# Performance work log

Measured on AMD Instinct MI355X. Metric: run time of the kernel, lower is better.

Reference implementation:

```python
import jax, jax.numpy as jnp
import numpy as np

N_TEXT = 80000
N_NON = 20000
N = N_TEXT + N_NON
E = 200000
EMB = 256
HID = 256
R = 500
V = 17
MDIM = 64
K = 4
NUM_ROUNDS = 2
NUM_REV_ROUNDS = 2


def setup_inputs():
    key = jax.random.key(0)
    ks = jax.random.split(key, 32)
    f = jnp.float32
    s = 0.05
    inp = {}
    inp["h_id_tensor"] = jax.random.randint(ks[0], (E,), 0, N)
    inp["r_id_tensor"] = jax.random.randint(ks[1], (E,), 0, R)
    inp["t_id_tensor"] = jax.random.randint(ks[2], (E,), 0, N)
    inp["q_emb"] = jax.random.normal(ks[3], (1, EMB), f)
    inp["entity_embs"] = jax.random.normal(ks[4], (N_TEXT, EMB), f)
    inp["num_non_text_entities"] = N_NON
    inp["relation_embs"] = jax.random.normal(ks[5], (R, EMB), f)
    inp["topic_entity_one_hot"] = (jax.random.uniform(ks[6], (N, 2)) < 0.01).astype(f)
    inp["node_motif_token_ids"] = jax.random.randint(ks[7], (N, K), 0, V)
    inp["node_motif_token_wts"] = jax.random.uniform(ks[8], (N, K), f)
    inp["triple_motif_token_ids"] = jax.random.randint(ks[9], (E, K), 0, V)
    inp["triple_motif_token_wts"] = jax.random.uniform(ks[10], (E, K), f)
    inp["non_text_emb"] = jax.random.normal(ks[11], (EMB,), f) * s
    me = jax.random.normal(ks[12], (V, MDIM), f) * s
    inp["motif_emb"] = me.at[0].set(0.0)  # padding_idx=0
    inp["gnn_self_w"] = jax.random.normal(ks[13], (MDIM, MDIM), f) * s
    inp["gnn_self_b"] = jnp.zeros((MDIM,), f)
    inp["gnn_msg_w"] = jax.random.normal(ks[14], (MDIM, MDIM), f) * s
    inp["gnn_msg_b"] = jnp.zeros((MDIM,), f)
    pos_dim = 2 + 2 * (NUM_ROUNDS + NUM_REV_ROUNDS)  # 10
    inp["nh_w"] = jax.random.normal(ks[15], (2 * EMB + 2 * MDIM, HID), f) * s
    inp["nh_b"] = jnp.zeros((HID,), f)
    inp["pos_w"] = jax.random.normal(ks[16], (2 * pos_dim, HID), f) * s
    inp["pos_b"] = jnp.zeros((HID,), f)
    inp["st_w"] = jax.random.normal(ks[17], (EMB + MDIM, HID), f) * s
    inp["st_b"] = jnp.zeros((HID,), f)
    inp["gate_w"] = jax.random.normal(ks[18], (EMB, 3), f) * s
    inp["gate_b"] = jnp.zeros((3,), f)
    inp["pred_w1"] = jax.random.normal(ks[19], (EMB + HID, HID), f) * s
    inp["pred_b1"] = jnp.zeros((HID,), f)
    inp["pred_w2"] = jax.random.normal(ks[20], (HID, 1), f) * s
    inp["pred_b2"] = jnp.zeros((1,), f)
    return inp


def _forward(h_id, r_id, t_id, q_emb, entity_embs, num_non_text, relation_embs,
             topic_oh, node_ids, node_wts, trip_ids, trip_wts,
             non_text_emb, motif_emb, gsw, gsb, gmw, gmb,
             nh_w, nh_b, pos_w, pos_b, st_w, st_b, gate_w, gate_b,
             pw1, pb1, pw2, pb2):
    n = entity_embs.shape[0] + num_non_text
    h_e = jnp.concatenate(
        [entity_embs,
         jnp.broadcast_to(non_text_emb[None, :], (num_non_text, entity_embs.shape[1]))],
        axis=0)  # [N, EMB]
    ones = jnp.ones((h_id.shape[0],), h_e.dtype)
    inv_fwd = 1.0 / jnp.clip(jax.ops.segment_sum(ones, t_id, num_segments=n), 1.0)[:, None]
    inv_rev = 1.0 / jnp.clip(jax.ops.segment_sum(ones, h_id, num_segments=n), 1.0)[:, None]

    def mean_agg(x, src, dst, inv):
        # PyG mean aggregation: mean of source features over incoming edges, 0 if none
        return jax.ops.segment_sum(x[src], dst, num_segments=n) * inv

    dde_list = []
    h = topic_oh
    for _ in range(NUM_ROUNDS):
        h = mean_agg(h, h_id, t_id, inv_fwd)
        dde_list.append(h)
    h = topic_oh
    for _ in range(NUM_REV_ROUNDS):
        h = mean_agg(h, t_id, h_id, inv_rev)
        dde_list.append(h)

    # ---- motif co-occurrence adjacency (vectorized form of the K x K loop) ----
    contrib = trip_wts[:, :, None] * trip_wts[:, None, :]                 # [E,K,K]
    valid = (trip_ids[:, :, None] > 0) & (trip_ids[:, None, :] > 0) & (contrib > 0)
    contrib = jnp.where(valid, contrib, 0.0)
    idx = (trip_ids[:, :, None] * V + trip_ids[:, None, :]).reshape(-1)
    adj = jnp.zeros((V * V,), contrib.dtype).at[idx].add(contrib.reshape(-1)).reshape(V, V)
    adj = 0.5 * (adj + adj.T) + jnp.eye(V, dtype=adj.dtype)
    adj = adj.at[0, :].set(0.0).at[:, 0].set(0.0).at[0, 0].set(1.0)
    adj = adj / jnp.clip(adj.sum(axis=1, keepdims=True), 1e-8)

    # ---- semantic GNN over the motif table ----
    ht = motif_emb
    for _ in range(1):  # semantic_gnn_num_layers = 1, dropout 0 (eval)
        msg = adj @ ht
        ht = ht + jax.nn.relu(ht @ gsw + gsb + msg @ gmw + gmb)

    node_motif_emb = (ht[node_ids] * node_wts[:, :, None]).sum(axis=1)    # [N,MDIM]
    triple_motif_emb = (ht[trip_ids] * trip_wts[:, :, None]).sum(axis=1)  # [E,MDIM]

    h_r = relation_embs[r_id]                                             # [E,EMB]
    h_nbr = jax.nn.relu(
        jnp.concatenate([h_e[h_id], h_e[t_id], node_motif_emb[h_id], node_motif_emb[t_id]],
                        axis=1) @ nh_w + nh_b)
    pos_feat = jnp.concatenate([topic_oh] + dde_list, axis=1)             # [N,10]
    h_pos = jax.nn.relu(
        jnp.concatenate([pos_feat[h_id], pos_feat[t_id]], axis=1) @ pos_w + pos_b)
    h_str = jax.nn.relu(jnp.concatenate([h_r, triple_motif_emb], axis=1) @ st_w + st_b)

    gate = jax.nn.softmax((q_emb @ gate_w + gate_b)[0])                   # [3]
    h_fused = gate[0] * h_nbr + gate[1] * h_pos + gate[2] * h_str
    pred_in = jnp.concatenate(
        [jnp.broadcast_to(q_emb, (h_r.shape[0], q_emb.shape[1])), h_fused], axis=1)
    return jax.nn.relu(pred_in @ pw1 + pb1) @ pw2 + pb2                   # [E,1]


def reference(h_id_tensor, r_id_tensor, t_id_tensor, q_emb, entity_embs,
              num_non_text_entities, relation_embs, topic_entity_one_hot,
              node_motif_token_ids, node_motif_token_wts,
              triple_motif_token_ids, triple_motif_token_wts,
              non_text_emb, motif_emb, gnn_self_w, gnn_self_b, gnn_msg_w, gnn_msg_b,
              nh_w, nh_b, pos_w, pos_b, st_w, st_b, gate_w, gate_b,
              pred_w1, pred_b1, pred_w2, pred_b2):
    return _forward(h_id_tensor, r_id_tensor, t_id_tensor, q_emb, entity_embs,
                    num_non_text_entities, relation_embs, topic_entity_one_hot,
                    node_motif_token_ids, node_motif_token_wts,
                    triple_motif_token_ids, triple_motif_token_wts,
                    non_text_emb, motif_emb, gnn_self_w, gnn_self_b, gnn_msg_w, gnn_msg_b,
                    nh_w, nh_b, pos_w, pos_b, st_w, st_b, gate_w, gate_b,
                    pred_w1, pred_b1, pred_w2, pred_b2)
```

## Files before the change

### kernel.cpp

```cpp
#include <hip/hip_runtime.h>
#include <hip/hip_bf16.h>

#define N_TEXT 80000
#define NTOT   100000
#define NE     200000
#define EMB    256
#define HID    256
#define VMOT   17
#define MDIM   64
#define KTOK   4

typedef unsigned short u16;
typedef unsigned int   u32;
typedef short short8 __attribute__((ext_vector_type(8)));
typedef float f32x4 __attribute__((ext_vector_type(4)));

#define O_INVF 0
#define O_INVR (NTOT)
#define O_POS  (2*NTOT)
#define O_ADJ  (12*NTOT)
#define O_HTB  (12*NTOT + 512)
#define O_GATE (12*NTOT + 1088)
#define O_CVEC (12*NTOT + 1104)
#define O_NME  (12*NTOT + 1360)
#define O_WSW  (O_NME + NTOT*32)
#define ZERO_FLOATS (12*NTOT + 512)

#define OW_A 0
#define OW_B 163840
#define OW_C 172032
#define OW_D 253952
#define SZ_W 319488
#define GA 20480
#define GB 1024
#define GC 10240
#define GD 8192
#define GTOT (GA+GB+GC+GD)

__device__ __forceinline__ u16 f2b(float f) {
  unsigned u = __float_as_uint(f);
  return (u16)((u + 0x7fffu + ((u >> 16) & 1u)) >> 16);
}
__device__ __forceinline__ float b2f(u16 v) {
  return __uint_as_float(((unsigned)v) << 16);
}
__device__ __forceinline__ short8 pack8(const float* f) {
  short8 v;
#pragma unroll
  for (int j = 0; j < 8; j++) v[j] = (short)f2b(f[j]);
  return v;
}

__global__ void k_zero(float* ws, int n) {
  int i = blockIdx.x * blockDim.x + threadIdx.x;
  if (i < n) ws[i] = 0.f;
}

__global__ void k_prep_w(const float* __restrict__ nh_w, const float* __restrict__ pos_w,
                         const float* __restrict__ st_w, const float* __restrict__ pw1,
                         float* __restrict__ ws) {
  int g = blockIdx.x * blockDim.x + threadIdx.x;
  if (g >= GTOT) return;
  int l, phase;
  if (g < GA) { l = g; phase = 0; }
  else if (g < GA + GB) { l = g - GA; phase = 1; }
  else if (g < GA + GB + GC) { l = g - GA - GB; phase = 2; }
  else { l = g - GA - GB - GC; phase = 3; }
  int c = l >> 10, r = l & 1023;
  int w = r >> 8, nt = (r >> 6) & 3, ln = r & 63;
  int col = w*64 + nt*16 + (ln & 15);
  int k0  = c*32 + ((ln >> 4) << 3);
  float f[8];
#pragma unroll
  for (int j = 0; j < 8; j++) {
    int k = k0 + j;
    float v = 0.f;
    if (phase == 0)      v = nh_w[k*256 + col];
    else if (phase == 1) { if (k < 10) v = pos_w[k*256 + col];
                           else if (k >= 16 && k < 26) v = pos_w[(k-6)*256 + col]; }
    else if (phase == 2) v = st_w[k*256 + col];
    else                 v = pw1[(256 + k)*256 + col];
    f[j] = v;
  }
  ((short8*)((u16*)(ws + O_WSW)))[g] = pack8(f);
}

__global__ void k_deg_dde1(const int* __restrict__ h_id, const int* __restrict__ t_id,
                           const float* __restrict__ topic, float* __restrict__ ws) {
  int e = blockIdx.x * blockDim.x + threadIdx.x;
  if (e >= NE) return;
  int h = h_id[e], t = t_id[e];
  atomicAdd(&ws[O_INVF + t], 1.0f);
  atomicAdd(&ws[O_INVR + h], 1.0f);
  float hx = topic[2*h], hy = topic[2*h + 1];
  float tx = topic[2*t], ty = topic[2*t + 1];
  if (hx != 0.f) atomicAdd(&ws[O_POS + t*10 + 2], hx);
  if (hy != 0.f) atomicAdd(&ws[O_POS + t*10 + 3], hy);
  if (tx != 0.f) atomicAdd(&ws[O_POS + h*10 + 6], tx);
  if (ty != 0.f) atomicAdd(&ws[O_POS + h*10 + 7], ty);
}

__global__ void k_prep_nodes(const float* __restrict__ topic, float* __restrict__ ws) {
  int n = blockIdx.x * blockDim.x + threadIdx.x;
  if (n >= NTOT) return;
  float invf = 1.0f / fmaxf(ws[O_INVF + n], 1.0f);
  float invr = 1.0f / fmaxf(ws[O_INVR + n], 1.0f);
  ws[O_INVF + n] = invf;
  ws[O_INVR + n] = invr;
  float* p = &ws[O_POS + n*10];
  p[0] = topic[2*n]; p[1] = topic[2*n + 1];
  p[2] *= invf; p[3] *= invf;
  p[6] *= invr; p[7] *= invr;
}

__global__ void k_dde2(const int* __restrict__ h_id, const int* __restrict__ t_id,
                       float* __restrict__ ws) {
  int e = blockIdx.x * blockDim.x + threadIdx.x;
  if (e >= NE) return;
  int h = h_id[e], t = t_id[e];
  float a = ws[O_POS + h*10 + 2], b = ws[O_POS + h*10 + 3];
  float c = ws[O_POS + t*10 + 6], d = ws[O_POS + t*10 + 7];
  if (a != 0.f) atomicAdd(&ws[O_POS + t*10 + 4], a);
  if (b != 0.f) atomicAdd(&ws[O_POS + t*10 + 5], b);
  if (c != 0.f) atomicAdd(&ws[O_POS + h*10 + 8], c);
  if (d != 0.f) atomicAdd(&ws[O_POS + h*10 + 9], d);
}

__global__ void k_dde2_scale(float* __restrict__ ws) {
  int n = blockIdx.x * blockDim.x + threadIdx.x;
  if (n >= NTOT) return;
  float invf = ws[O_INVF + n], invr = ws[O_INVR + n];
  float* p = &ws[O_POS + n*10];
  p[4] *= invf; p[5] *= invf;
  p[8] *= invr; p[9] *= invr;
}

__global__ void k_adj(const int* __restrict__ tids, const float* __restrict__ twts,
                      float* __restrict__ ws) {
  __shared__ float sadj[4*304];
  for (int i = threadIdx.x; i < 4*304; i += blockDim.x) sadj[i] = 0.f;
  __syncthreads();
  int wbase = (threadIdx.x >> 6) * 304;
  int e = blockIdx.x * blockDim.x + threadIdx.x;
  if (e < NE) {
    int id[KTOK]; float w[KTOK];
#pragma unroll
    for (int k = 0; k < KTOK; k++) { id[k] = tids[e*KTOK + k]; w[k] = twts[e*KTOK + k]; }
#pragma unroll
    for (int i = 0; i < KTOK; i++)
#pragma unroll
      for (int j = 0; j < KTOK; j++) {
        float c = w[i] * w[j];
        if (id[i] > 0 && id[j] > 0 && c > 0.f)
          atomicAdd(&sadj[wbase + id[i]*VMOT + id[j]], c);
      }
  }
  __syncthreads();
  for (int i = threadIdx.x; i < VMOT*VMOT; i += blockDim.x) {
    float v = sadj[i] + sadj[304 + i] + sadj[608 + i] + sadj[912 + i];
    if (v != 0.f) atomicAdd(&ws[O_ADJ + i], v);
  }
}

__global__ void k_motif_gate(const float* __restrict__ mo, const float* __restrict__ gsw,
                             const float* __restrict__ gsb, const float* __restrict__ gmw,
                             const float* __restrict__ gmb, const float* __restrict__ q,
                             const float* __restrict__ gate_w, const float* __restrict__ gate_b,
                             const float* __restrict__ pw1, const float* __restrict__ pb1,
                             float* __restrict__ ws) {
  int t = threadIdx.x;
  if (blockIdx.x == 0) {
    __shared__ float A[VMOT*VMOT];
    __shared__ float Bm[VMOT*VMOT];
    __shared__ float inv_row[VMOT];
    __shared__ float smo[VMOT*MDIM];
    __shared__ float sm[VMOT*MDIM];
    for (int i = t; i < VMOT*VMOT; i += blockDim.x) A[i] = ws[O_ADJ + i];
    for (int i = t; i < VMOT*MDIM; i += blockDim.x) smo[i] = mo[i];
    __syncthreads();
    for (int i = t; i < VMOT*VMOT; i += blockDim.x) {
      int r = i / VMOT, c = i % VMOT;
      float v = 0.5f * (A[i] + A[c*VMOT + r]) + (r == c ? 1.f : 0.f);
      if (r == 0 || c == 0) v = (r == 0 && c == 0) ? 1.f : 0.f;
      Bm[i] = v;
    }
    __syncthreads();
    if (t < VMOT) {
      float s = 0.f;
      for (int c = 0; c < VMOT; c++) s += Bm[t*VMOT + c];
      inv_row[t] = 1.f / fmaxf(s, 1e-8f);
    }
    __syncthreads();
    for (int i = t; i < VMOT*MDIM; i += blockDim.x) {
      int v = i / MDIM, d = i % MDIM;
      float s = 0.f;
      for (int u = 0; u < VMOT; u++) s += Bm[v*VMOT + u] * smo[u*MDIM + d];
      sm[i] = s * inv_row[v];
    }
    __syncthreads();
    for (int i = t; i < VMOT*MDIM; i += blockDim.x) {
      int v = i / MDIM, d = i % MDIM;
      float a = gsb[d] + gmb[d];
      for (int m = 0; m < MDIM; m++)
        a += smo[v*MDIM + m] * gsw[m*MDIM + d] + sm[v*MDIM + m] * gmw[m*MDIM + d];
      ((u16*)(ws + O_HTB))[i] = f2b(smo[i] + fmaxf(a, 0.f));
    }
  } else {
    __shared__ float sq[EMB];
    __shared__ float red[3];
    sq[t] = q[t];
    if (t < 3) red[t] = 0.f;
    __syncthreads();
    float s = pb1[t];
    for (int i = 0; i < EMB; i++) s += sq[i] * pw1[i*HID + t];
    ws[O_CVEC + t] = s;
    atomicAdd(&red[0], sq[t] * gate_w[t*3 + 0]);
    atomicAdd(&red[1], sq[t] * gate_w[t*3 + 1]);
    atomicAdd(&red[2], sq[t] * gate_w[t*3 + 2]);
    __syncthreads();
    if (t == 0) {
      float l0 = red[0] + gate_b[0], l1 = red[1] + gate_b[1], l2 = red[2] + gate_b[2];
      float mx = fmaxf(l0, fmaxf(l1, l2));
      float e0 = expf(l0 - mx), e1 = expf(l1 - mx), e2 = expf(l2 - mx);
      float inv = 1.f / (e0 + e1 + e2);
      ws[O_GATE + 0] = e0 * inv; ws[O_GATE + 1] = e1 * inv; ws[O_GATE + 2] = e2 * inv;
    }
  }
}

__global__ void k_nme(const int* __restrict__ nids, const float* __restrict__ nwts,
                      float* __restrict__ ws) {
  __shared__ u16 sht[VMOT*MDIM];
  for (int i = threadIdx.x; i < (VMOT*MDIM)/2; i += blockDim.x)
    ((u32*)sht)[i] = ((const u32*)(ws + O_HTB))[i];
  __syncthreads();
  int gid = blockIdx.x * blockDim.x + threadIdx.x;
  if (gid >= NTOT * 8) return;
  int n = gid >> 3, d0 = (gid & 7) * 8;
  int4   iv = ((const int4*)nids)[n];
  float4 wv = ((const float4*)nwts)[n];
  int   id[4] = {iv.x, iv.y, iv.z, iv.w};
  float w[4]  = {wv.x, wv.y, wv.z, wv.w};
  float f[8];
#pragma unroll
  for (int j = 0; j < 8; j++) {
    float s = 0.f;
#pragma unroll
    for (int k = 0; k < 4; k++) s += w[k] * b2f(sht[id[k]*MDIM + d0 + j]);
    f[j] = s;
  }
  ((short8*)((u16*)(ws + O_NME)))[gid] = pack8(f);
}

__global__ __launch_bounds__(256, 2) void k_edge_mfma(
    const int* __restrict__ h_id, const int* __restrict__ r_id, const int* __restrict__ t_id,
    const float* __restrict__ ent, const float* __restrict__ rel, const float* __restrict__ nte,
    const int* __restrict__ tids, const float* __restrict__ twts,
    const float* __restrict__ nh_b, const float* __restrict__ pos_b,
    const float* __restrict__ st_b, const float* __restrict__ pw2,
    const float* __restrict__ pb2,
    const float* __restrict__ ws, float* __restrict__ out) {
  __shared__ __align__(16) u16 sX[64*32];
  __shared__ __align__(16) u16 sW[8192];
  __shared__ __align__(16) u16 sF[8*64*32];
  __shared__ float sOut[64];
  __shared__ int sh[64], stt[64], sr[64];

  const int tid = threadIdx.x;
  const int wv = tid >> 6, ln = tid & 63;
  const int lm = ln & 15, lq = ln >> 4;
  const int cb = wv * 64;
  const int e0 = blockIdx.x * 64;
  const int srow = tid >> 2, sks = tid & 3;

  if (tid < 64) {
    sh[tid]  = h_id[e0 + tid];
    stt[tid] = t_id[e0 + tid];
    sr[tid]  = r_id[e0 + tid];
    sOut[tid] = 0.f;
  }
  const float g0 = ws[O_GATE + 0], g1 = ws[O_GATE + 1], g2 = ws[O_GATE + 2];
  const u16* Wsw = (const u16*)(ws + O_WSW);
  const u16* WA = Wsw + OW_A;
  const u16* WB = Wsw + OW_B;
  const u16* WC = Wsw + OW_C;
  const u16* WD = Wsw + OW_D;
  const u16* nmeb = (const u16*)(ws + O_NME);
  const u16* htb  = (const u16*)(ws + O_HTB);
  const int4   tiv = ((const int4*)tids)[e0 + srow];
  const float4 twv = ((const float4*)twts)[e0 + srow];
  __syncthreads();

  f32x4 acc[4][4];
  float fused[4][4][4];
#pragma unroll
  for (int mt = 0; mt < 4; mt++)
#pragma unroll
    for (int nt = 0; nt < 4; nt++) {
      acc[mt][nt] = (f32x4){0.f, 0.f, 0.f, 0.f};
#pragma unroll
      for (int r = 0; r < 4; r++) fused[mt][nt][r] = 0.f;
    }

#define LOADW(W, c)                                                      \
  { const u16* p = (W) + (c)*8192 + tid*8;                               \
    wreg[0] = *(const short8*)(p);                                       \
    wreg[1] = *(const short8*)(p + 2048);                                \
    wreg[2] = *(const short8*)(p + 4096);                                \
    wreg[3] = *(const short8*)(p + 6144); }

#define STOREW()                                                         \
  { *(short8*)&sW[tid*8]        = wreg[0];                               \
    *(short8*)&sW[2048 + tid*8] = wreg[1];                               \
    *(short8*)&sW[4096 + tid*8] = wreg[2];                               \
    *(short8*)&sW[6144 + tid*8] = wreg[3]; }

#define MFMA_STEP()                                                      \
  { short8 a[4], b[4];                                                   \
    _Pragma("unroll")                                                    \
    for (int mt = 0; mt < 4; mt++)                                       \
      a[mt] = *(const short8*)&sX[(mt*16 + lm)*32 + lq*8];               \
    _Pragma("unroll")                                                    \
    for (int nt = 0; nt < 4; nt++)                                       \
      b[nt] = *(const short8*)&sW[wv*2048 + nt*512 + ln*8];              \
    _Pragma("unroll")                                                    \
    for (int mt = 0; mt < 4; mt++)                                       \
      _Pragma("unroll")                                                  \
      for (int nt = 0; nt < 4; nt++)                                     \
        acc[mt][nt] = __builtin_amdgcn_mfma_f32_16x16x32_bf16(a[mt], b[nt], acc[mt][nt], 0, 0, 0); }

  short8 wreg[4];

  {
    float4 fa, fb; short8 xs;
    auto loadA = [&](int kc) {
      int kk = kc + sks*8;
      if (kk < 512) {
        int node = (kk < 256) ? sh[srow] : stt[srow];
        int k2 = kk & 255;
        const float* src = (node < N_TEXT) ? &ent[(size_t)node*256 + k2] : &nte[k2];
        fa = *(const float4*)src; fb = *(const float4*)(src + 4);
      } else {
        int node = (kk < 576) ? sh[srow] : stt[srow];
        xs = *(const short8*)&nmeb[node*64 + ((kk - 512) & 63)];
      }
    };
    loadA(0); LOADW(WA, 0);
    for (int c = 0; c < 20; c++) {
      if (c*32 < 512) {
        float f[8] = {fa.x, fa.y, fa.z, fa.w, fb.x, fb.y, fb.z, fb.w};
        *(short8*)&sX[srow*32 + sks*8] = pack8(f);
      } else {
        *(short8*)&sX[srow*32 + sks*8] = xs;
      }
      STOREW();
      __syncthreads();
      if (c < 19) { loadA((c+1)*32); LOADW(WA, c+1); }
      MFMA_STEP();
      __syncthreads();
    }
  }
#pragma unroll
  for (int nt = 0; nt < 4; nt++) {
    float bb = nh_b[cb + nt*16 + lm];
#pragma unroll
    for (int mt = 0; mt < 4; mt++)
#pragma unroll
      for (int r = 0; r < 4; r++) {
        fused[mt][nt][r] += g0 * fmaxf(acc[mt][nt][r] + bb, 0.f);
        acc[mt][nt][r] = 0.f;
      }
  }

  {
    LOADW(WB, 0);
    int node_h = sh[srow], node_t = stt[srow];
    float f[8];
#pragma unroll
    for (int j = 0; j < 8; j++) {
      int kk = sks*8 + j;
      float v = 0.f;
      if (kk < 10) v = ws[O_POS + node_h*10 + kk];
      else if (kk >= 16 && kk < 26) v = ws[O_POS + node_t*10 + kk - 16];
      f[j] = v;
    }
    *(short8*)&sX[srow*32 + sks*8] = pack8(f);
    STOREW();
    __syncthreads();
    MFMA_STEP();
    __syncthreads();
  }
#pragma unroll
  for (int nt = 0; nt < 4; nt++) {
    float bb = pos_b[cb + nt*16 + lm];
#pragma unroll
    for (int mt = 0; mt < 4; mt++)
#pragma unroll
      for (int r = 0; r < 4; r++) {
        fused[mt][nt][r] += g1 * fmaxf(acc[mt][nt][r] + bb, 0.f);
        acc[mt][nt][r] = 0.f;
      }
  }

  {
    float4 fa, fb; short8 hs0, hs1, hs2, hs3;
    auto loadC = [&](int kc) {
      int kk = kc + sks*8;
      if (kk < 256) {
        const float* src = &rel[(size_t)sr[srow]*256 + kk];
        fa = *(const float4*)src; fb = *(const float4*)(src + 4);
      } else {
        int d0 = kk - 256;
        hs0 = *(const short8*)&htb[tiv.x*64 + d0];
        hs1 = *(const short8*)&htb[tiv.y*64 + d0];
        hs2 = *(const short8*)&htb[tiv.z*64 + d0];
        hs3 = *(const short8*)&htb[tiv.w*64 + d0];
      }
    };
    loadC(0); LOADW(WC, 0);
    for (int c = 0; c < 10; c++) {
      if (c < 8) {
        float f[8] = {fa.x, fa.y, fa.z, fa.w, fb.x, fb.y, fb.z, fb.w};
        *(short8*)&sX[srow*32 + sks*8] = pack8(f);
      } else {
        float f[8];
#pragma unroll
        for (int j = 0; j < 8; j++)
          f[j] = twv.x * b2f((u16)hs0[j]) + twv.y * b2f((u16)hs1[j])
               + twv.z * b2f((u16)hs2[j]) + twv.w * b2f((u16)hs3[j]);
        *(short8*)&sX[srow*32 + sks*8] = pack8(f);
      }
      STOREW();
      __syncthreads();
      if (c < 9) { loadC((c+1)*32); LOADW(WC, c+1); }
      MFMA_STEP();
      __syncthreads();
    }
  }
#pragma unroll
  for (int nt = 0; nt < 4; nt++) {
    float bb = st_b[cb + nt*16 + lm];
#pragma unroll
    for (int mt = 0; mt < 4; mt++)
#pragma unroll
      for (int r = 0; r < 4; r++) {
        fused[mt][nt][r] += g2 * fmaxf(acc[mt][nt][r] + bb, 0.f);
        acc[mt][nt][r] = 0.f;
      }
  }

  LOADW(WD, 0);
#pragma unroll
  for (int mt = 0; mt < 4; mt++)
#pragma unroll
    for (int nt = 0; nt < 4; nt++) {
      int col = cb + nt*16 + lm;
      int base = (col >> 5)*2048 + (col & 31);
#pragma unroll
      for (int r = 0; r < 4; r++)
        sF[base + (mt*16 + lq*4 + r)*32] = f2b(fused[mt][nt][r]);
    }

  for (int c = 0; c < 8; c++) {
    STOREW();
    __syncthreads();
    if (c < 7) LOADW(WD, c+1);
    {
      short8 a[4], b[4];
#pragma unroll
      for (int mt = 0; mt < 4; mt++)
        a[mt] = *(const short8*)&sF[c*2048 + (mt*16 + lm)*32 + lq*8];
#pragma unroll
      for (int nt = 0; nt < 4; nt++)
        b[nt] = *(const short8*)&sW[wv*2048 + nt*512 + ln*8];
#pragma unroll
      for (int mt = 0; mt < 4; mt++)
#pragma unroll
        for (int nt = 0; nt < 4; nt++)
          acc[mt][nt] = __builtin_amdgcn_mfma_f32_16x16x32_bf16(a[mt], b[nt], acc[mt][nt], 0, 0, 0);
    }
    __syncthreads();
  }

  {
    float cv[4], p2[4];
#pragma unroll
    for (int nt = 0; nt < 4; nt++) {
      int col = cb + nt*16 + lm;
      cv[nt] = ws[O_CVEC + col];
      p2[nt] = pw2[col];
    }
#pragma unroll
    for (int mt = 0; mt < 4; mt++)
#pragma unroll
      for (int r = 0; r < 4; r++) {
        float s = 0.f;
#pragma unroll
        for (int nt = 0; nt < 4; nt++)
          s += fmaxf(acc[mt][nt][r] + cv[nt], 0.f) * p2[nt];
#pragma unroll
        for (int off = 1; off < 16; off <<= 1)
          s += __shfl_xor(s, off, 64);
        if (lm == 0) atomicAdd(&sOut[mt*16 + lq*4 + r], s);
      }
  }
  __syncthreads();
  if (tid < 64) out[e0 + tid] = sOut[tid] + pb2[0];
#undef LOADW
#undef STOREW
#undef MFMA_STEP
}

extern "C" void kernel_launch(void* const* d_in, const int* in_sizes, int n_in,
                              void* d_out, int out_size, void* d_ws, size_t ws_size,
                              hipStream_t stream) {
  (void)in_sizes; (void)n_in; (void)out_size; (void)ws_size;
  const int*   h_id   = (const int*)  d_in[0];
  const int*   r_id   = (const int*)  d_in[1];
  const int*   t_id   = (const int*)  d_in[2];
  const float* q      = (const float*)d_in[3];
  const float* ent    = (const float*)d_in[4];
  const float* rel    = (const float*)d_in[6];
  const float* topic  = (const float*)d_in[7];
  const int*   nids   = (const int*)  d_in[8];
  const float* nwts   = (const float*)d_in[9];
  const int*   tids   = (const int*)  d_in[10];
  const float* twts   = (const float*)d_in[11];
  const float* nte    = (const float*)d_in[12];
  const float* mo     = (const float*)d_in[13];
  const float* gsw    = (const float*)d_in[14];
  const float* gsb    = (const float*)d_in[15];
  const float* gmw    = (const float*)d_in[16];
  const float* gmb    = (const float*)d_in[17];
  const float* nh_w   = (const float*)d_in[18];
  const float* nh_b   = (const float*)d_in[19];
  const float* pos_w  = (const float*)d_in[20];
  const float* pos_b  = (const float*)d_in[21];
  const float* st_w   = (const float*)d_in[22];
  const float* st_b   = (const float*)d_in[23];
  const float* gate_w = (const float*)d_in[24];
  const float* gate_b = (const float*)d_in[25];
  const float* pw1    = (const float*)d_in[26];
  const float* pb1    = (const float*)d_in[27];
  const float* pw2    = (const float*)d_in[28];
  const float* pb2    = (const float*)d_in[29];
  float* ws  = (float*)d_ws;
  float* out = (float*)d_out;

  k_zero<<<(ZERO_FLOATS + 255)/256, 256, 0, stream>>>(ws, ZERO_FLOATS);
  k_prep_w<<<(GTOT + 255)/256, 256, 0, stream>>>(nh_w, pos_w, st_w, pw1, ws);
  k_deg_dde1<<<(NE + 255)/256, 256, 0, stream>>>(h_id, t_id, topic, ws);
  k_prep_nodes<<<(NTOT + 255)/256, 256, 0, stream>>>(topic, ws);
  k_dde2<<<(NE + 255)/256, 256, 0, stream>>>(h_id, t_id, ws);
  k_dde2_scale<<<(NTOT + 255)/256, 256, 0, stream>>>(ws);
  k_adj<<<(NE + 255)/256, 256, 0, stream>>>(tids, twts, ws);
  k_motif_gate<<<2, 256, 0, stream>>>(mo, gsw, gsb, gmw, gmb, q, gate_w, gate_b, pw1, pb1, ws);
  k_nme<<<(NTOT*8 + 255)/256, 256, 0, stream>>>(nids, nwts, ws);
  k_edge_mfma<<<NE/64, 256, 0, stream>>>(h_id, r_id, t_id, ent, rel, nte, tids, twts,
                                         nh_b, pos_b, st_b, pw2, pb2, ws, out);
}
```

Before: 533.5 us.

## Fuse preprocessing kernels and load MFMA operands directly from global memory

Result: slower. 710.9 us (+33.2%).

```diff
diff --git a/kernel.cpp b/kernel.cpp
--- a/kernel.cpp
+++ b/kernel.cpp
@@ -25,12 +25,12 @@
 #define O_NME  (12*NTOT + 1360)
 #define O_WSW  (O_NME + NTOT*32)
 #define ZERO_FLOATS (12*NTOT + 512)
+#define Z4 (ZERO_FLOATS/4)
 
 #define OW_A 0
 #define OW_B 163840
 #define OW_C 172032
 #define OW_D 253952
-#define SZ_W 319488
 #define GA 20480
 #define GB 1024
 #define GC 10240
@@ -44,22 +44,22 @@
 __device__ __forceinline__ float b2f(u16 v) {
   return __uint_as_float(((unsigned)v) << 16);
 }
-__device__ __forceinline__ short8 pack8(const float* f) {
-  short8 v;
-#pragma unroll
-  for (int j = 0; j < 8; j++) v[j] = (short)f2b(f[j]);
-  return v;
-}
-
-__global__ void k_zero(float* ws, int n) {
-  int i = blockIdx.x * blockDim.x + threadIdx.x;
-  if (i < n) ws[i] = 0.f;
-}
-
-__global__ void k_prep_w(const float* __restrict__ nh_w, const float* __restrict__ pos_w,
-                         const float* __restrict__ st_w, const float* __restrict__ pw1,
-                         float* __restrict__ ws) {
+__device__ __forceinline__ short8 pack8f(const float* f) {
+  union { u32 u[4]; short8 s; } o;
+#pragma unroll
+  for (int i = 0; i < 4; i++) {
+    __hip_bfloat162 b = __float22bfloat162_rn(float2{f[2*i], f[2*i+1]});
+    o.u[i] = *reinterpret_cast<u32*>(&b);
+  }
+  return o.s;
+}
+
+__global__ void k_prep(const float* __restrict__ nh_w, const float* __restrict__ pos_w,
+                       const float* __restrict__ st_w, const float* __restrict__ pw1,
+                       float* __restrict__ ws) {
   int g = blockIdx.x * blockDim.x + threadIdx.x;
+  if (g < Z4) { ((float4*)ws)[g] = make_float4(0.f, 0.f, 0.f, 0.f); return; }
+  g -= Z4;
   if (g >= GTOT) return;
   int l, phase;
   if (g < GA) { l = g; phase = 0; }
@@ -82,67 +82,28 @@
     else                 v = pw1[(256 + k)*256 + col];
     f[j] = v;
   }
-  ((short8*)((u16*)(ws + O_WSW)))[g] = pack8(f);
-}
-
-__global__ void k_deg_dde1(const int* __restrict__ h_id, const int* __restrict__ t_id,
-                           const float* __restrict__ topic, float* __restrict__ ws) {
-  int e = blockIdx.x * blockDim.x + threadIdx.x;
-  if (e >= NE) return;
-  int h = h_id[e], t = t_id[e];
-  atomicAdd(&ws[O_INVF + t], 1.0f);
-  atomicAdd(&ws[O_INVR + h], 1.0f);
-  float hx = topic[2*h], hy = topic[2*h + 1];
-  float tx = topic[2*t], ty = topic[2*t + 1];
-  if (hx != 0.f) atomicAdd(&ws[O_POS + t*10 + 2], hx);
-  if (hy != 0.f) atomicAdd(&ws[O_POS + t*10 + 3], hy);
-  if (tx != 0.f) atomicAdd(&ws[O_POS + h*10 + 6], tx);
-  if (ty != 0.f) atomicAdd(&ws[O_POS + h*10 + 7], ty);
-}
-
-__global__ void k_prep_nodes(const float* __restrict__ topic, float* __restrict__ ws) {
-  int n = blockIdx.x * blockDim.x + threadIdx.x;
-  if (n >= NTOT) return;
-  float invf = 1.0f / fmaxf(ws[O_INVF + n], 1.0f);
-  float invr = 1.0f / fmaxf(ws[O_INVR + n], 1.0f);
-  ws[O_INVF + n] = invf;
-  ws[O_INVR + n] = invr;
-  float* p = &ws[O_POS + n*10];
-  p[0] = topic[2*n]; p[1] = topic[2*n + 1];
-  p[2] *= invf; p[3] *= invf;
-  p[6] *= invr; p[7] *= invr;
-}
-
-__global__ void k_dde2(const int* __restrict__ h_id, const int* __restrict__ t_id,
-                       float* __restrict__ ws) {
-  int e = blockIdx.x * blockDim.x + threadIdx.x;
-  if (e >= NE) return;
-  int h = h_id[e], t = t_id[e];
-  float a = ws[O_POS + h*10 + 2], b = ws[O_POS + h*10 + 3];
-  float c = ws[O_POS + t*10 + 6], d = ws[O_POS + t*10 + 7];
-  if (a != 0.f) atomicAdd(&ws[O_POS + t*10 + 4], a);
-  if (b != 0.f) atomicAdd(&ws[O_POS + t*10 + 5], b);
-  if (c != 0.f) atomicAdd(&ws[O_POS + h*10 + 8], c);
-  if (d != 0.f) atomicAdd(&ws[O_POS + h*10 + 9], d);
-}
-
-__global__ void k_dde2_scale(float* __restrict__ ws) {
-  int n = blockIdx.x * blockDim.x + threadIdx.x;
-  if (n >= NTOT) return;
-  float invf = ws[O_INVF + n], invr = ws[O_INVR + n];
-  float* p = &ws[O_POS + n*10];
-  p[4] *= invf; p[5] *= invf;
-  p[8] *= invr; p[9] *= invr;
-}
-
-__global__ void k_adj(const int* __restrict__ tids, const float* __restrict__ twts,
-                      float* __restrict__ ws) {
+  ((short8*)((u16*)(ws + O_WSW)))[g] = pack8f(f);
+}
+
+__global__ void k_deg_dde1_adj(const int* __restrict__ h_id, const int* __restrict__ t_id,
+                               const float* __restrict__ topic,
+                               const int* __restrict__ tids, const float* __restrict__ twts,
+                               float* __restrict__ ws) {
   __shared__ float sadj[4*304];
   for (int i = threadIdx.x; i < 4*304; i += blockDim.x) sadj[i] = 0.f;
   __syncthreads();
   int wbase = (threadIdx.x >> 6) * 304;
   int e = blockIdx.x * blockDim.x + threadIdx.x;
   if (e < NE) {
+    int h = h_id[e], t = t_id[e];
+    atomicAdd(&ws[O_INVF + t], 1.0f);
+    atomicAdd(&ws[O_INVR + h], 1.0f);
+    float hx = topic[2*h], hy = topic[2*h + 1];
+    float tx = topic[2*t], ty = topic[2*t + 1];
+    if (hx != 0.f) atomicAdd(&ws[O_POS + t*10 + 2], hx);
+    if (hy != 0.f) atomicAdd(&ws[O_POS + t*10 + 3], hy);
+    if (tx != 0.f) atomicAdd(&ws[O_POS + h*10 + 6], tx);
+    if (ty != 0.f) atomicAdd(&ws[O_POS + h*10 + 7], ty);
     int id[KTOK]; float w[KTOK];
 #pragma unroll
     for (int k = 0; k < KTOK; k++) { id[k] = tids[e*KTOK + k]; w[k] = twts[e*KTOK + k]; }
@@ -162,23 +123,35 @@
   }
 }
 
-__global__ void k_motif_gate(const float* __restrict__ mo, const float* __restrict__ gsw,
-                             const float* __restrict__ gsb, const float* __restrict__ gmw,
-                             const float* __restrict__ gmb, const float* __restrict__ q,
-                             const float* __restrict__ gate_w, const float* __restrict__ gate_b,
-                             const float* __restrict__ pw1, const float* __restrict__ pb1,
-                             float* __restrict__ ws) {
+#define NPN_BLOCKS ((NTOT + 255)/256)
+__global__ void k_pnm(const float* __restrict__ topic, const float* __restrict__ mo,
+                      const float* __restrict__ gsw, const float* __restrict__ gsb,
+                      const float* __restrict__ gmw, const float* __restrict__ gmb,
+                      const float* __restrict__ q, const float* __restrict__ gate_w,
+                      const float* __restrict__ gate_b, const float* __restrict__ pw1,
+                      const float* __restrict__ pb1, float* __restrict__ ws) {
   int t = threadIdx.x;
-  if (blockIdx.x == 0) {
+  if (blockIdx.x < NPN_BLOCKS) {
+    int n = blockIdx.x * 256 + t;
+    if (n >= NTOT) return;
+    float invf = 1.0f / fmaxf(ws[O_INVF + n], 1.0f);
+    float invr = 1.0f / fmaxf(ws[O_INVR + n], 1.0f);
+    ws[O_INVF + n] = invf;
+    ws[O_INVR + n] = invr;
+    float* p = &ws[O_POS + n*10];
+    p[0] = topic[2*n]; p[1] = topic[2*n + 1];
+    p[2] *= invf; p[3] *= invf;
+    p[6] *= invr; p[7] *= invr;
+  } else if (blockIdx.x == NPN_BLOCKS) {
     __shared__ float A[VMOT*VMOT];
     __shared__ float Bm[VMOT*VMOT];
     __shared__ float inv_row[VMOT];
     __shared__ float smo[VMOT*MDIM];
     __shared__ float sm[VMOT*MDIM];
-    for (int i = t; i < VMOT*VMOT; i += blockDim.x) A[i] = ws[O_ADJ + i];
-    for (int i = t; i < VMOT*MDIM; i += blockDim.x) smo[i] = mo[i];
+    for (int i = t; i < VMOT*VMOT; i += 256) A[i] = ws[O_ADJ + i];
+    for (int i = t; i < VMOT*MDIM; i += 256) smo[i] = mo[i];
     __syncthreads();
-    for (int i = t; i < VMOT*VMOT; i += blockDim.x) {
+    for (int i = t; i < VMOT*VMOT; i += 256) {
       int r = i / VMOT, c = i % VMOT;
       float v = 0.5f * (A[i] + A[c*VMOT + r]) + (r == c ? 1.f : 0.f);
       if (r == 0 || c == 0) v = (r == 0 && c == 0) ? 1.f : 0.f;
@@ -191,14 +164,14 @@
       inv_row[t] = 1.f / fmaxf(s, 1e-8f);
     }
     __syncthreads();
-    for (int i = t; i < VMOT*MDIM; i += blockDim.x) {
+    for (int i = t; i < VMOT*MDIM; i += 256) {
       int v = i / MDIM, d = i % MDIM;
       float s = 0.f;
       for (int u = 0; u < VMOT; u++) s += Bm[v*VMOT + u] * smo[u*MDIM + d];
       sm[i] = s * inv_row[v];
     }
     __syncthreads();
-    for (int i = t; i < VMOT*MDIM; i += blockDim.x) {
+    for (int i = t; i < VMOT*MDIM; i += 256) {
       int v = i / MDIM, d = i % MDIM;
       float a = gsb[d] + gmb[d];
       for (int m = 0; m < MDIM; m++)
@@ -228,31 +201,46 @@
   }
 }
 
-__global__ void k_nme(const int* __restrict__ nids, const float* __restrict__ nwts,
-                      float* __restrict__ ws) {
+__global__ void k_dde2(const int* __restrict__ h_id, const int* __restrict__ t_id,
+                       float* __restrict__ ws) {
+  int e = blockIdx.x * blockDim.x + threadIdx.x;
+  if (e >= NE) return;
+  int h = h_id[e], t = t_id[e];
+  float a = ws[O_POS + h*10 + 2], b = ws[O_POS + h*10 + 3];
+  float c = ws[O_POS + t*10 + 6], d = ws[O_POS + t*10 + 7];
+  if (a != 0.f) atomicAdd(&ws[O_POS + t*10 + 4], a);
+  if (b != 0.f) atomicAdd(&ws[O_POS + t*10 + 5], b);
+  if (c != 0.f) atomicAdd(&ws[O_POS + h*10 + 8], c);
+  if (d != 0.f) atomicAdd(&ws[O_POS + h*10 + 9], d);
+}
+
+__global__ void k_scale_nme(const int* __restrict__ nids, const float* __restrict__ nwts,
+                            float* __restrict__ ws) {
   __shared__ u16 sht[VMOT*MDIM];
   for (int i = threadIdx.x; i < (VMOT*MDIM)/2; i += blockDim.x)
     ((u32*)sht)[i] = ((const u32*)(ws + O_HTB))[i];
   __syncthreads();
   int gid = blockIdx.x * blockDim.x + threadIdx.x;
+  if (gid < NTOT) {
+    float invf = ws[O_INVF + gid], invr = ws[O_INVR + gid];
+    float* p = &ws[O_POS + gid*10];
+    p[4] *= invf; p[5] *= invf;
+    p[8] *= invr; p[9] *= invr;
+  }
   if (gid >= NTOT * 8) return;
   int n = gid >> 3, d0 = (gid & 7) * 8;
   int4   iv = ((const int4*)nids)[n];
   float4 wv = ((const float4*)nwts)[n];
-  int   id[4] = {iv.x, iv.y, iv.z, iv.w};
-  float w[4]  = {wv.x, wv.y, wv.z, wv.w};
   float f[8];
 #pragma unroll
   for (int j = 0; j < 8; j++) {
-    float s = 0.f;
-#pragma unroll
-    for (int k = 0; k < 4; k++) s += w[k] * b2f(sht[id[k]*MDIM + d0 + j]);
-    f[j] = s;
-  }
-  ((short8*)((u16*)(ws + O_NME)))[gid] = pack8(f);
-}
-
-__global__ __launch_bounds__(256, 2) void k_edge_mfma(
+    f[j] = wv.x * b2f(sht[iv.x*MDIM + d0 + j]) + wv.y * b2f(sht[iv.y*MDIM + d0 + j])
+         + wv.z * b2f(sht[iv.z*MDIM + d0 + j]) + wv.w * b2f(sht[iv.w*MDIM + d0 + j]);
+  }
+  ((short8*)((u16*)(ws + O_NME)))[gid] = pack8f(f);
+}
+
+__global__ __launch_bounds__(256, 3) void k_edge_mfma(
     const int* __restrict__ h_id, const int* __restrict__ r_id, const int* __restrict__ t_id,
     const float* __restrict__ ent, const float* __restrict__ rel, const float* __restrict__ nte,
     const int* __restrict__ tids, const float* __restrict__ twts,
@@ -260,226 +248,192 @@
     const float* __restrict__ st_b, const float* __restrict__ pw2,
     const float* __restrict__ pb2,
     const float* __restrict__ ws, float* __restrict__ out) {
-  __shared__ __align__(16) u16 sX[64*32];
-  __shared__ __align__(16) u16 sW[8192];
-  __shared__ __align__(16) u16 sF[8*64*32];
+  __shared__ __align__(16) u16 sF[16384];
   __shared__ float sOut[64];
-  __shared__ int sh[64], stt[64], sr[64];
 
   const int tid = threadIdx.x;
   const int wv = tid >> 6, ln = tid & 63;
   const int lm = ln & 15, lq = ln >> 4;
   const int cb = wv * 64;
   const int e0 = blockIdx.x * 64;
-  const int srow = tid >> 2, sks = tid & 3;
-
-  if (tid < 64) {
-    sh[tid]  = h_id[e0 + tid];
-    stt[tid] = t_id[e0 + tid];
-    sr[tid]  = r_id[e0 + tid];
-    sOut[tid] = 0.f;
+
+  if (tid < 64) sOut[tid] = 0.f;
+
+  int nh[4], ntl[4], nr[4];
+#pragma unroll
+  for (int mt = 0; mt < 4; mt++) {
+    int e = e0 + mt*16 + lm;
+    nh[mt] = h_id[e]; ntl[mt] = t_id[e]; nr[mt] = r_id[e];
   }
   const float g0 = ws[O_GATE + 0], g1 = ws[O_GATE + 1], g2 = ws[O_GATE + 2];
-  const u16* Wsw = (const u16*)(ws + O_WSW);
-  const u16* WA = Wsw + OW_A;
-  const u16* WB = Wsw + OW_B;
-  const u16* WC = Wsw + OW_C;
-  const u16* WD = Wsw + OW_D;
+  const u16* blob = (const u16*)(ws + O_WSW);
   const u16* nmeb = (const u16*)(ws + O_NME);
   const u16* htb  = (const u16*)(ws + O_HTB);
-  const int4   tiv = ((const int4*)tids)[e0 + srow];
-  const float4 twv = ((const float4*)twts)[e0 + srow];
-  __syncthreads();
 
   f32x4 acc[4][4];
-  float fused[4][4][4];
 #pragma unroll
   for (int mt = 0; mt < 4; mt++)
 #pragma unroll
-    for (int nt = 0; nt < 4; nt++) {
-      acc[mt][nt] = (f32x4){0.f, 0.f, 0.f, 0.f};
-#pragma unroll
-      for (int r = 0; r < 4; r++) fused[mt][nt][r] = 0.f;
-    }
-
-#define LOADW(W, c)                                                      \
-  { const u16* p = (W) + (c)*8192 + tid*8;                               \
-    wreg[0] = *(const short8*)(p);                                       \
-    wreg[1] = *(const short8*)(p + 2048);                                \
-    wreg[2] = *(const short8*)(p + 4096);                                \
-    wreg[3] = *(const short8*)(p + 6144); }
-
-#define STOREW()                                                         \
-  { *(short8*)&sW[tid*8]        = wreg[0];                               \
-    *(short8*)&sW[2048 + tid*8] = wreg[1];                               \
-    *(short8*)&sW[4096 + tid*8] = wreg[2];                               \
-    *(short8*)&sW[6144 + tid*8] = wreg[3]; }
-
-#define MFMA_STEP()                                                      \
-  { short8 a[4], b[4];                                                   \
-    _Pragma("unroll")                                                    \
-    for (int mt = 0; mt < 4; mt++)                                       \
-      a[mt] = *(const short8*)&sX[(mt*16 + lm)*32 + lq*8];               \
-    _Pragma("unroll")                                                    \
-    for (int nt = 0; nt < 4; nt++)                                       \
-      b[nt] = *(const short8*)&sW[wv*2048 + nt*512 + ln*8];              \
-    _Pragma("unroll")                                                    \
-    for (int mt = 0; mt < 4; mt++)                                       \
-      _Pragma("unroll")                                                  \
-      for (int nt = 0; nt < 4; nt++)                                     \
-        acc[mt][nt] = __builtin_amdgcn_mfma_f32_16x16x32_bf16(a[mt], b[nt], acc[mt][nt], 0, 0, 0); }
-
-  short8 wreg[4];
-
-  {
-    float4 fa, fb; short8 xs;
-    auto loadA = [&](int kc) {
-      int kk = kc + sks*8;
-      if (kk < 512) {
-        int node = (kk < 256) ? sh[srow] : stt[srow];
-        int k2 = kk & 255;
-        const float* src = (node < N_TEXT) ? &ent[(size_t)node*256 + k2] : &nte[k2];
-        fa = *(const float4*)src; fb = *(const float4*)(src + 4);
-      } else {
-        int node = (kk < 576) ? sh[srow] : stt[srow];
-        xs = *(const short8*)&nmeb[node*64 + ((kk - 512) & 63)];
-      }
-    };
-    loadA(0); LOADW(WA, 0);
-    for (int c = 0; c < 20; c++) {
-      if (c*32 < 512) {
-        float f[8] = {fa.x, fa.y, fa.z, fa.w, fb.x, fb.y, fb.z, fb.w};
-        *(short8*)&sX[srow*32 + sks*8] = pack8(f);
-      } else {
-        *(short8*)&sX[srow*32 + sks*8] = xs;
-      }
-      STOREW();
-      __syncthreads();
-      if (c < 19) { loadA((c+1)*32); LOADW(WA, c+1); }
-      MFMA_STEP();
-      __syncthreads();
-    }
+    for (int nt = 0; nt < 4; nt++) acc[mt][nt] = (f32x4){0.f, 0.f, 0.f, 0.f};
+
+  auto bload = [&](int bc, short8 (&b)[4]) {
+#pragma unroll
+    for (int nt = 0; nt < 4; nt++)
+      b[nt] = *(const short8*)&blob[(size_t)bc*8192 + wv*2048 + nt*512 + ln*8];
+  };
+  auto mfma16 = [&](short8 (&a)[4], short8 (&b)[4]) {
+#pragma unroll
+    for (int mt = 0; mt < 4; mt++)
+#pragma unroll
+      for (int nt = 0; nt < 4; nt++)
+        acc[mt][nt] = __builtin_amdgcn_mfma_f32_16x16x32_bf16(a[mt], b[nt], acc[mt][nt], 0, 0, 0);
+  };
+
+#pragma unroll 2
+  for (int c = 0; c < 8; c++) {
+    short8 a[4], b[4];
+#pragma unroll
+    for (int mt = 0; mt < 4; mt++) {
+      int node = nh[mt];
+      const float* p = ((node < N_TEXT) ? &ent[(size_t)node*256] : nte) + c*32 + lq*8;
+      float4 v0 = *(const float4*)p, v1 = *(const float4*)(p + 4);
+      float f[8] = {v0.x, v0.y, v0.z, v0.w, v1.x, v1.y, v1.z, v1.w};
+      a[mt] = pack8f(f);
+    }
+    bload(c, b); mfma16(a, b);
+  }
+#pragma unroll 2
+  for (int c = 0; c < 8; c++) {
+    short8 a[4], b[4];
+#pragma unroll
+    for (int mt = 0; mt < 4; mt++) {
+      int node = ntl[mt];
+      const float* p = ((node < N_TEXT) ? &ent[(size_t)node*256] : nte) + c*32 + lq*8;
+      float4 v0 = *(const float4*)p, v1 = *(const float4*)(p + 4);
+      float f[8] = {v0.x, v0.y, v0.z, v0.w, v1.x, v1.y, v1.z, v1.w};
+      a[mt] = pack8f(f);
+    }
+    bload(8 + c, b); mfma16(a, b);
+  }
+#pragma unroll
+  for (int c = 0; c < 2; c++) {
+    short8 a[4], b[4];
+#pragma unroll
+    for (int mt = 0; mt < 4; mt++)
+      a[mt] = *(const short8*)&nmeb[(size_t)nh[mt]*64 + c*32 + lq*8];
+    bload(16 + c, b); mfma16(a, b);
+  }
+#pragma unroll
+  for (int c = 0; c < 2; c++) {
+    short8 a[4], b[4];
+#pragma unroll
+    for (int mt = 0; mt < 4; mt++)
+      a[mt] = *(const short8*)&nmeb[(size_t)ntl[mt]*64 + c*32 + lq*8];
+    bload(18 + c, b); mfma16(a, b);
   }
 #pragma unroll
   for (int nt = 0; nt < 4; nt++) {
-    float bb = nh_b[cb + nt*16 + lm];
+    int col = cb + nt*16 + lm;
+    float bb = nh_b[col];
+    int base = (col >> 5)*2048 + (col & 31);
 #pragma unroll
     for (int mt = 0; mt < 4; mt++)
 #pragma unroll
       for (int r = 0; r < 4; r++) {
-        fused[mt][nt][r] += g0 * fmaxf(acc[mt][nt][r] + bb, 0.f);
+        sF[base + (mt*16 + lq*4 + r)*32] = f2b(g0 * fmaxf(acc[mt][nt][r] + bb, 0.f));
         acc[mt][nt][r] = 0.f;
       }
   }
 
   {
-    LOADW(WB, 0);
-    int node_h = sh[srow], node_t = stt[srow];
-    float f[8];
-#pragma unroll
-    for (int j = 0; j < 8; j++) {
-      int kk = sks*8 + j;
-      float v = 0.f;
-      if (kk < 10) v = ws[O_POS + node_h*10 + kk];
-      else if (kk >= 16 && kk < 26) v = ws[O_POS + node_t*10 + kk - 16];
-      f[j] = v;
-    }
-    *(short8*)&sX[srow*32 + sks*8] = pack8(f);
-    STOREW();
-    __syncthreads();
-    MFMA_STEP();
-    __syncthreads();
+    short8 a[4], b[4];
+#pragma unroll
+    for (int mt = 0; mt < 4; mt++) {
+      int node = (lq < 2) ? nh[mt] : ntl[mt];
+      int k0 = (lq & 1) * 8;
+      const float* p = &ws[O_POS + (size_t)node*10 + k0];
+      float2 v0 = *(const float2*)p,       v1 = *(const float2*)(p + 2);
+      float2 v2 = *(const float2*)(p + 4), v3 = *(const float2*)(p + 6);
+      float f[8] = {v0.x, v0.y, v1.x, v1.y, v2.x, v2.y, v3.x, v3.y};
+#pragma unroll
+      for (int j = 0; j < 8; j++) if (k0 + j >= 10) f[j] = 0.f;
+      a[mt] = pack8f(f);
+    }
+    bload((OW_B/8192), b); mfma16(a, b);
   }
 #pragma unroll
   for (int nt = 0; nt < 4; nt++) {
-    float bb = pos_b[cb + nt*16 + lm];
+    int col = cb + nt*16 + lm;
+    float bb = pos_b[col];
+    int base = (col >> 5)*2048 + (col & 31);
 #pragma unroll
     for (int mt = 0; mt < 4; mt++)
 #pragma unroll
       for (int r = 0; r < 4; r++) {
-        fused[mt][nt][r] += g1 * fmaxf(acc[mt][nt][r] + bb, 0.f);
+        u16* p = &sF[base + (mt*16 + lq*4 + r)*32];
+        *p = f2b(b2f(*p) + g1 * fmaxf(acc[mt][nt][r] + bb, 0.f));
         acc[mt][nt][r] = 0.f;
       }
   }
 
-  {
-    float4 fa, fb; short8 hs0, hs1, hs2, hs3;
-    auto loadC = [&](int kc) {
-      int kk = kc + sks*8;
-      if (kk < 256) {
-        const float* src = &rel[(size_t)sr[srow]*256 + kk];
-        fa = *(const float4*)src; fb = *(const float4*)(src + 4);
-      } else {
-        int d0 = kk - 256;
-        hs0 = *(const short8*)&htb[tiv.x*64 + d0];
-        hs1 = *(const short8*)&htb[tiv.y*64 + d0];
-        hs2 = *(const short8*)&htb[tiv.z*64 + d0];
-        hs3 = *(const short8*)&htb[tiv.w*64 + d0];
-      }
-    };
-    loadC(0); LOADW(WC, 0);
-    for (int c = 0; c < 10; c++) {
-      if (c < 8) {
-        float f[8] = {fa.x, fa.y, fa.z, fa.w, fb.x, fb.y, fb.z, fb.w};
-        *(short8*)&sX[srow*32 + sks*8] = pack8(f);
-      } else {
-        float f[8];
-#pragma unroll
-        for (int j = 0; j < 8; j++)
-          f[j] = twv.x * b2f((u16)hs0[j]) + twv.y * b2f((u16)hs1[j])
-               + twv.z * b2f((u16)hs2[j]) + twv.w * b2f((u16)hs3[j]);
-        *(short8*)&sX[srow*32 + sks*8] = pack8(f);
-      }
-      STOREW();
-      __syncthreads();
-      if (c < 9) { loadC((c+1)*32); LOADW(WC, c+1); }
-      MFMA_STEP();
-      __syncthreads();
-    }
+#pragma unroll 2
+  for (int c = 0; c < 8; c++) {
+    short8 a[4], b[4];
+#pragma unroll
+    for (int mt = 0; mt < 4; mt++) {
+      const float* p = &rel[(size_t)nr[mt]*256 + c*32 + lq*8];
+      float4 v0 = *(const float4*)p, v1 = *(const float4*)(p + 4);
+      float f[8] = {v0.x, v0.y, v0.z, v0.w, v1.x, v1.y, v1.z, v1.w};
+      a[mt] = pack8f(f);
+    }
+    bload(OW_C/8192 + c, b); mfma16(a, b);
+  }
+#pragma unroll
+  for (int c = 0; c < 2; c++) {
+    short8 a[4], b[4];
+#pragma unroll
+    for (int mt = 0; mt < 4; mt++) {
+      int e = e0 + mt*16 + lm;
+      int4   iv  = ((const int4*)tids)[e];
+      float4 wv4 = ((const float4*)twts)[e];
+      int d0 = c*32 + lq*8;
+      short8 h0 = *(const short8*)&htb[iv.x*64 + d0];
+      short8 h1 = *(const short8*)&htb[iv.y*64 + d0];
+      short8 h2 = *(const short8*)&htb[iv.z*64 + d0];
+      short8 h3 = *(const short8*)&htb[iv.w*64 + d0];
+      float f[8];
+#pragma unroll
+      for (int j = 0; j < 8; j++)
+        f[j] = wv4.x * b2f((u16)h0[j]) + wv4.y * b2f((u16)h1[j])
+             + wv4.z * b2f((u16)h2[j]) + wv4.w * b2f((u16)h3[j]);
+      a[mt] = pack8f(f);
+    }
+    bload(OW_C/8192 + 8 + c, b); mfma16(a, b);
   }
 #pragma unroll
   for (int nt = 0; nt < 4; nt++) {
-    float bb = st_b[cb + nt*16 + lm];
+    int col = cb + nt*16 + lm;
+    float bb = st_b[col];
+    int base = (col >> 5)*2048 + (col & 31);
 #pragma unroll
     for (int mt = 0; mt < 4; mt++)
 #pragma unroll
       for (int r = 0; r < 4; r++) {
-        fused[mt][nt][r] += g2 * fmaxf(acc[mt][nt][r] + bb, 0.f);
+        u16* p = &sF[base + (mt*16 + lq*4 + r)*32];
+        *p = f2b(b2f(*p) + g2 * fmaxf(acc[mt][nt][r] + bb, 0.f));
         acc[mt][nt][r] = 0.f;
       }
   }
 
-  LOADW(WD, 0);
-#pragma unroll
-  for (int mt = 0; mt < 4; mt++)
-#pragma unroll
-    for (int nt = 0; nt < 4; nt++) {
-      int col = cb + nt*16 + lm;
-      int base = (col >> 5)*2048 + (col & 31);
-#pragma unroll
-      for (int r = 0; r < 4; r++)
-        sF[base + (mt*16 + lq*4 + r)*32] = f2b(fused[mt][nt][r]);
-    }
-
+  __syncthreads();
+
+#pragma unroll 2
   for (int c = 0; c < 8; c++) {
-    STOREW();
-    __syncthreads();
-    if (c < 7) LOADW(WD, c+1);
-    {
-      short8 a[4], b[4];
-#pragma unroll
-      for (int mt = 0; mt < 4; mt++)
-        a[mt] = *(const short8*)&sF[c*2048 + (mt*16 + lm)*32 + lq*8];
-#pragma unroll
-      for (int nt = 0; nt < 4; nt++)
-        b[nt] = *(const short8*)&sW[wv*2048 + nt*512 + ln*8];
-#pragma unroll
-      for (int mt = 0; mt < 4; mt++)
-#pragma unroll
-        for (int nt = 0; nt < 4; nt++)
-          acc[mt][nt] = __builtin_amdgcn_mfma_f32_16x16x32_bf16(a[mt], b[nt], acc[mt][nt], 0, 0, 0);
-    }
-    __syncthreads();
+    short8 a[4], b[4];
+#pragma unroll
+    for (int mt = 0; mt < 4; mt++)
+      a[mt] = *(const short8*)&sF[c*2048 + (mt*16 + lm)*32 + lq*8];
+    bload(OW_D/8192 + c, b); mfma16(a, b);
   }
 
   {
@@ -506,9 +460,6 @@
   }
   __syncthreads();
   if (tid < 64) out[e0 + tid] = sOut[tid] + pb2[0];
-#undef LOADW
-#undef STOREW
-#undef MFMA_STEP
 }
 
 extern "C" void kernel_launch(void* const* d_in, const int* in_sizes, int n_in,
@@ -532,7 +483,6 @@
   const float* gsb    = (const float*)d_in[15];
   const float* gmw    = (const float*)d_in[16];
   const float* gmb    = (const float*)d_in[17];
-  const float* nh_w   = (const float*)d_in[18];
   const float* nh_b   = (const float*)d_in[19];
   const float* pos_w  = (const float*)d_in[20];
   const float* pos_b  = (const float*)d_in[21];
@@ -544,18 +494,16 @@
   const float* pb1    = (const float*)d_in[27];
   const float* pw2    = (const float*)d_in[28];
   const float* pb2    = (const float*)d_in[29];
+  const float* nh_w   = (const float*)d_in[18];
   float* ws  = (float*)d_ws;
   float* out = (float*)d_out;
 
-  k_zero<<<(ZERO_FLOATS + 255)/256, 256, 0, stream>>>(ws, ZERO_FLOATS);
-  k_prep_w<<<(GTOT + 255)/256, 256, 0, stream>>>(nh_w, pos_w, st_w, pw1, ws);
-  k_deg_dde1<<<(NE + 255)/256, 256, 0, stream>>>(h_id, t_id, topic, ws);
-  k_prep_nodes<<<(NTOT + 255)/256, 256, 0, stream>>>(topic, ws);
+  k_prep<<<(Z4 + GTOT + 255)/256, 256, 0, stream>>>(nh_w, pos_w, st_w, pw1, ws);
+  k_deg_dde1_adj<<<(NE + 255)/256, 256, 0, stream>>>(h_id, t_id, topic, tids, twts, ws);
+  k_pnm<<<NPN_BLOCKS + 2, 256, 0, stream>>>(topic, mo, gsw, gsb, gmw, gmb,
+                                            q, gate_w, gate_b, pw1, pb1, ws);
   k_dde2<<<(NE + 255)/256, 256, 0, stream>>>(h_id, t_id, ws);
-  k_dde2_scale<<<(NTOT + 255)/256, 256, 0, stream>>>(ws);
-  k_adj<<<(NE + 255)/256, 256, 0, stream>>>(tids, twts, ws);
-  k_motif_gate<<<2, 256, 0, stream>>>(mo, gsw, gsb, gmw, gmb, q, gate_w, gate_b, pw1, pb1, ws);
-  k_nme<<<(NTOT*8 + 255)/256, 256, 0, stream>>>(nids, nwts, ws);
+  k_scale_nme<<<(NTOT*8 + 255)/256, 256, 0, stream>>>(nids, nwts, ws);
   k_edge_mfma<<<NE/64, 256, 0, stream>>>(h_id, r_id, t_id, ent, rel, nte, tids, twts,
                                          nh_b, pos_b, st_b, pw2, pb2, ws, out);
 }
```
